# Kernel optimization log

Hardware: AMD Instinct MI355X
Metric: run time of the kernel (lower is better)

Reference implementation:

```python
import jax, jax.numpy as jnp
import numpy as np

N_NODES = 50000
N_EDGES = 800000
N_FIELDS = 4
N_MESH = 8
HIDDEN = 128
IN_CH = N_FIELDS * 1 + N_MESH  # 12


def _w(key, shape, scale=0.05):
    return jax.random.normal(key, shape, dtype=jnp.float32) * scale


def setup_inputs() -> dict:
    key = jax.random.key(0)
    ks = jax.random.split(key, 20)
    inp = {
        "F_0": jax.random.normal(ks[0], (N_NODES, 1, N_FIELDS), dtype=jnp.float32),
        "meshfield": jax.random.normal(ks[1], (N_NODES, N_MESH), dtype=jnp.float32),
        "edge_index": jax.random.randint(ks[2], (2, N_EDGES), 0, N_NODES, dtype=jnp.int32),
        "n_timesteps": 8,
        # encoder SAGEConv 1: in 12 -> 128 ; SAGEConv 2: 128 -> 128
        "enc1_Wl": _w(ks[3], (HIDDEN, IN_CH)), "enc1_bl": jnp.zeros((HIDDEN,), jnp.float32), "enc1_Wr": _w(ks[4], (HIDDEN, IN_CH)),
        "enc2_Wl": _w(ks[5], (HIDDEN, HIDDEN)), "enc2_bl": jnp.zeros((HIDDEN,), jnp.float32), "enc2_Wr": _w(ks[6], (HIDDEN, HIDDEN)),
        # decoder SAGEConv 1 & 2: 128 -> 128
        "dec1_Wl": _w(ks[7], (HIDDEN, HIDDEN)), "dec1_bl": jnp.zeros((HIDDEN,), jnp.float32), "dec1_Wr": _w(ks[8], (HIDDEN, HIDDEN)),
        "dec2_Wl": _w(ks[9], (HIDDEN, HIDDEN)), "dec2_bl": jnp.zeros((HIDDEN,), jnp.float32), "dec2_Wr": _w(ks[10], (HIDDEN, HIDDEN)),
        # output head: 128 -> n_fields
        "lin_W": _w(ks[11], (N_FIELDS, HIDDEN)), "lin_b": jnp.zeros((N_FIELDS,), jnp.float32),
    }
    return inp


def sage_conv(x, src, dst, Wl, bl, Wr, n_nodes):
    # PyG SAGEConv: out = lin_l(mean_j x_j) + lin_r(x_i); lin_l has bias, lin_r does not.
    msg = x[src]                                             # [E, C] gather
    agg = jax.ops.segment_sum(msg, dst, num_segments=n_nodes)
    cnt = jax.ops.segment_sum(jnp.ones((src.shape[0], 1), x.dtype), dst, num_segments=n_nodes)
    agg = agg / jnp.maximum(cnt, 1.0)                        # scatter-mean
    return agg @ Wl.T + bl + x @ Wr.T


def reference(F_0, meshfield, edge_index, n_timesteps,
              enc1_Wl, enc1_bl, enc1_Wr, enc2_Wl, enc2_bl, enc2_Wr,
              dec1_Wl, dec1_bl, dec1_Wr, dec2_Wl, dec2_bl, dec2_Wr,
              lin_W, lin_b):
    n = F_0.shape[0]
    src, dst = edge_index[0], edge_index[1]
    relu = jax.nn.relu
    F_prev = F_0  # [N, n_prev=1, n_fields]
    outs = []
    for _ in range(int(n_timesteps)):
        x_prev = F_prev[:, -1]                               # [N, n_fields]
        x = jnp.concatenate([F_prev.reshape(n, -1), meshfield], axis=1)  # [N, 12]
        # encoder GraphSAGE (act between layers, none after last)
        h = relu(sage_conv(x, src, dst, enc1_Wl, enc1_bl, enc1_Wr, n))
        h = sage_conv(h, src, dst, enc2_Wl, enc2_bl, enc2_Wr, n)
        h = relu(h)                                          # self.act after encoder
        # decoder GraphSAGE
        h = relu(sage_conv(h, src, dst, dec1_Wl, dec1_bl, dec1_Wr, n))
        h = sage_conv(h, src, dst, dec2_Wl, dec2_bl, dec2_Wr, n)
        h = relu(h)                                          # self.act after decoder
        x_new = x_prev + h @ lin_W.T + lin_b                 # residual update
        outs.append(x_new[:, None, :])
        # recurrence uses detached prediction (x.detach() in torch)
        F_prev = jnp.concatenate([F_prev[:, 1:], jax.lax.stop_gradient(x_new)[:, None, :]], axis=1)
    return jnp.concatenate(outs, axis=1)                     # [N, n_timesteps, n_fields]
```

## Files before the change

### kernel.cpp

```cpp
#include <hip/hip_runtime.h>


typedef __attribute__((ext_vector_type(8))) short short8;
typedef __attribute__((ext_vector_type(8))) unsigned short ushort8;
typedef __attribute__((ext_vector_type(4))) float f32x4;

static __device__ __forceinline__ float b2f(unsigned short u) {
  return __uint_as_float(((unsigned int)u) << 16);
}
static __device__ __forceinline__ unsigned short f2bf(float f) {
  unsigned int u = __float_as_uint(f);
  u += 0x7FFFu + ((u >> 16) & 1u);
  return (unsigned short)(u >> 16);
}


__global__ void count_deg_kernel(const int* __restrict__ dst, int* __restrict__ cnt, int E) {
  int e = blockIdx.x * blockDim.x + threadIdx.x;
  if (e < E) atomicAdd(&cnt[dst[e]], 1);
}

__global__ void rdeg_kernel(const int* __restrict__ cnt, float* __restrict__ rdeg, int N) {
  int n = blockIdx.x * blockDim.x + threadIdx.x;
  if (n < N) rdeg[n] = 1.0f / fmaxf((float)cnt[n], 1.0f);
}

__global__ __launch_bounds__(1024) void scan_kernel(const int* __restrict__ cnt,
                                                    int* __restrict__ row_ptr, int n) {
  __shared__ int sums[1024];
  int tid = threadIdx.x;
  int seg = (n + 1023) >> 10;
  int i0 = tid * seg;
  int i1 = i0 + seg; if (i1 > n) i1 = n;
  int s = 0;
  for (int i = i0; i < i1; ++i) s += cnt[i];
  sums[tid] = s;
  __syncthreads();
  for (int off = 1; off < 1024; off <<= 1) {
    int t = (tid >= off) ? sums[tid - off] : 0;
    __syncthreads();
    sums[tid] += t;
    __syncthreads();
  }
  int run = (tid == 0) ? 0 : sums[tid - 1];
  for (int i = i0; i < i1; ++i) { run += cnt[i]; row_ptr[i + 1] = run; }
  if (tid == 0) row_ptr[0] = 0;
}

__global__ void fill_csr_kernel(const int* __restrict__ src, const int* __restrict__ dst,
                                const int* __restrict__ row_ptr, int* __restrict__ cursor,
                                int* __restrict__ col, int E) {
  int e = blockIdx.x * blockDim.x + threadIdx.x;
  if (e < E) {
    int d = dst[e];
    int p = atomicAdd(&cursor[d], 1);
    col[row_ptr[d] + p] = src[e];
  }
}

__global__ void f2bf_kernel(const float* __restrict__ src, unsigned short* __restrict__ dst, int n) {
  int i = blockIdx.x * blockDim.x + threadIdx.x;
  if (i < n) dst[i] = f2bf(src[i]);
}


__global__ void build_xcat_kernel(const float* __restrict__ xprev, const float* __restrict__ mesh,
                                  float* __restrict__ xcat, int N) {
  int g = blockIdx.x * blockDim.x + threadIdx.x;
  if (g < N * 12) {
    int n = g / 12, c = g % 12;
    xcat[g] = (c < 4) ? xprev[n * 4 + c] : mesh[n * 8 + (c - 4)];
  }
}

__global__ void agg12_kernel(const float* __restrict__ feat, float* __restrict__ out,
                             const int* __restrict__ row_ptr, const int* __restrict__ col,
                             const float* __restrict__ rdeg, int N) {
  int g = blockIdx.x * blockDim.x + threadIdx.x;
  int node = g >> 4;
  int d = g & 15;
  if (node >= N || d >= 12) return;
  int j0 = row_ptr[node], j1 = row_ptr[node + 1];
  float acc = 0.0f;
  for (int j = j0; j < j1; ++j) acc += feat[col[j] * 12 + d];
  out[node * 12 + d] = acc * rdeg[node];
}

__global__ void agg128_kernel(const unsigned short* __restrict__ feat,
                              unsigned short* __restrict__ out,
                              const int* __restrict__ row_ptr, const int* __restrict__ col,
                              const float* __restrict__ rdeg, int N) {
  int g = blockIdx.x * blockDim.x + threadIdx.x;
  int node = g >> 4;
  int d = g & 15;
  if (node >= N) return;
  int j0 = row_ptr[node], j1 = row_ptr[node + 1];
  float acc[8] = {};
  int j = j0;
  for (; j + 2 <= j1; j += 2) {
    int s0 = col[j], s1 = col[j + 1];
    ushort8 v0 = *(const ushort8*)&feat[s0 * 128 + d * 8];
    ushort8 v1 = *(const ushort8*)&feat[s1 * 128 + d * 8];
#pragma unroll
    for (int r = 0; r < 8; ++r) acc[r] += b2f(v0[r]) + b2f(v1[r]);
  }
  if (j < j1) {
    ushort8 v0 = *(const ushort8*)&feat[col[j] * 128 + d * 8];
#pragma unroll
    for (int r = 0; r < 8; ++r) acc[r] += b2f(v0[r]);
  }
  float rd = rdeg[node];
  ushort8 o;
#pragma unroll
  for (int r = 0; r < 8; ++r) o[r] = f2bf(acc[r] * rd);
  *(ushort8*)&out[node * 128 + d * 8] = o;
}

__global__ __launch_bounds__(256) void gemm12_kernel(
    const float* __restrict__ agg, const float* __restrict__ x,
    const float* __restrict__ Wl, const float* __restrict__ Wr,
    const float* __restrict__ bl, unsigned short* __restrict__ out, int N) {
  __shared__ float Ws[24][128];
  __shared__ float As[16][24];
  int tid = threadIdx.x;
  int nb = blockIdx.x * 16;
  for (int i = tid; i < 1536; i += 256) {
    int o = i / 12, k = i % 12;
    Ws[k][o] = Wl[i];
    Ws[12 + k][o] = Wr[i];
  }
  for (int i = tid; i < 192; i += 256) {
    int n = i / 12, k = i % 12;
    int gn = nb + n; if (gn > N - 1) gn = N - 1;
    As[n][k] = agg[gn * 12 + k];
    As[n][12 + k] = x[gn * 12 + k];
  }
  __syncthreads();
  int nl = tid >> 4;
  int og = tid & 15;
  float acc[8] = {};
#pragma unroll
  for (int k = 0; k < 24; ++k) {
    float a = As[nl][k];
    float4 w0 = *(const float4*)&Ws[k][og * 8];
    float4 w1 = *(const float4*)&Ws[k][og * 8 + 4];
    acc[0] += a * w0.x; acc[1] += a * w0.y; acc[2] += a * w0.z; acc[3] += a * w0.w;
    acc[4] += a * w1.x; acc[5] += a * w1.y; acc[6] += a * w1.z; acc[7] += a * w1.w;
  }
  int gn = nb + nl;
  if (gn < N) {
#pragma unroll
    for (int j = 0; j < 8; ++j) {
      float v = acc[j] + bl[og * 8 + j];
      out[gn * 128 + og * 8 + j] = f2bf(fmaxf(v, 0.0f));
    }
  }
}

__global__ __launch_bounds__(256) void gemm128_mfma_kernel(
    const unsigned short* __restrict__ agg, const unsigned short* __restrict__ x,
    const unsigned short* __restrict__ Wlb, const unsigned short* __restrict__ Wrb,
    const float* __restrict__ bl, unsigned short* __restrict__ out, int N) {
  int tid = threadIdx.x;
  int wave = tid >> 6;
  int lane = tid & 63;
  int nb = blockIdx.x * 128 + wave * 32;
  int l15 = lane & 15;
  int lk = (lane >> 4) * 8;

  f32x4 acc[2][8] = {};
  int r0 = nb + l15;      if (r0 > N - 1) r0 = N - 1;
  int r1 = nb + 16 + l15; if (r1 > N - 1) r1 = N - 1;

#pragma unroll
  for (int ks = 0; ks < 8; ++ks) {
    const unsigned short* As = (ks < 4) ? agg : x;
    const unsigned short* Ws = (ks < 4) ? Wlb : Wrb;
    int ko = (ks & 3) * 32 + lk;
    short8 a0 = *(const short8*)&As[r0 * 128 + ko];
    short8 a1 = *(const short8*)&As[r1 * 128 + ko];
#pragma unroll
    for (int ot = 0; ot < 8; ++ot) {
      short8 b = *(const short8*)&Ws[(ot * 16 + l15) * 128 + ko];
      acc[0][ot] = __builtin_amdgcn_mfma_f32_16x16x32_bf16(a0, b, acc[0][ot], 0, 0, 0);
      acc[1][ot] = __builtin_amdgcn_mfma_f32_16x16x32_bf16(a1, b, acc[1][ot], 0, 0, 0);
    }
  }

  int crow = (lane >> 4) * 4;
#pragma unroll
  for (int ot = 0; ot < 8; ++ot) {
    int gcol = ot * 16 + l15;
    float bv = bl[gcol];
#pragma unroll
    for (int mt = 0; mt < 2; ++mt) {
#pragma unroll
      for (int r = 0; r < 4; ++r) {
        int grow = nb + mt * 16 + crow + r;
        if (grow < N) {
          float v = fmaxf(acc[mt][ot][r] + bv, 0.0f);
          out[grow * 128 + gcol] = f2bf(v);
        }
      }
    }
  }
}

__global__ __launch_bounds__(256) void lin_kernel(
    const unsigned short* __restrict__ h, const float* __restrict__ linW,
    const float* __restrict__ linb, float* __restrict__ xprev,
    float* __restrict__ out, int N, int T, int t) {
  __shared__ float hs[64][132];
  __shared__ float Wls[4][132];
  int tid = threadIdx.x;
  int nb = blockIdx.x * 64;
  for (int i = tid; i < 512; i += 256) Wls[i >> 7][i & 127] = linW[i];
  for (int i = tid; i < 1024; i += 256) {
    int n = i >> 4, c = i & 15;
    int gn = nb + n; if (gn > N - 1) gn = N - 1;
    ushort8 v = *(const ushort8*)&h[gn * 128 + c * 8];
#pragma unroll
    for (int r = 0; r < 8; ++r) hs[n][c * 8 + r] = b2f(v[r]);
  }
  __syncthreads();
  int nl = tid >> 2, o = tid & 3;
  float acc = 0.0f;
#pragma unroll 8
  for (int k = 0; k < 128; k += 4) {
    float4 hv = *(const float4*)&hs[nl][k];
    float4 wv = *(const float4*)&Wls[o][k];
    acc += hv.x * wv.x + hv.y * wv.y + hv.z * wv.z + hv.w * wv.w;
  }
  int gn = nb + nl;
  if (gn < N) {
    float v = xprev[gn * 4 + o] + acc + linb[o];
    out[(gn * T + t) * 4 + o] = v;
    xprev[gn * 4 + o] = v;
  }
}

extern "C" void kernel_launch(void* const* d_in, const int* in_sizes, int n_in,
                              void* d_out, int out_size, void* d_ws, size_t ws_size,
                              hipStream_t stream) {
  const float* F0   = (const float*)d_in[0];
  const float* mesh = (const float*)d_in[1];
  const int*   eidx = (const int*)d_in[2];
  const float* e1Wl = (const float*)d_in[4];
  const float* e1bl = (const float*)d_in[5];
  const float* e1Wr = (const float*)d_in[6];
  const float* e2Wl = (const float*)d_in[7];
  const float* e2bl = (const float*)d_in[8];
  const float* e2Wr = (const float*)d_in[9];
  const float* d1Wl = (const float*)d_in[10];
  const float* d1bl = (const float*)d_in[11];
  const float* d1Wr = (const float*)d_in[12];
  const float* d2Wl = (const float*)d_in[13];
  const float* d2bl = (const float*)d_in[14];
  const float* d2Wr = (const float*)d_in[15];
  const float* linW = (const float*)d_in[16];
  const float* linb = (const float*)d_in[17];

  const int N = in_sizes[0] / 4;
  const int E = in_sizes[2] / 2;
  const int T = out_size / (N * 4);
  const int* src = eidx;
  const int* dst = eidx + E;

  size_t off = 0;
  auto alloc = [&](size_t bytes) -> void* {
    void* p = (char*)d_ws + off;
    off += (bytes + 511) & ~(size_t)511;
    return p;
  };
  int*   cnt     = (int*)alloc((size_t)N * 4);
  int*   row_ptr = (int*)alloc((size_t)(N + 1) * 4);
  int*   cursor  = (int*)alloc((size_t)N * 4);
  int*   col     = (int*)alloc((size_t)E * 4);
  float* rdeg    = (float*)alloc((size_t)N * 4);
  float* xprev   = (float*)alloc((size_t)N * 4 * 4);
  float* xcat    = (float*)alloc((size_t)N * 12 * 4);
  float* agg12b  = (float*)alloc((size_t)N * 12 * 4);
  unsigned short* h1   = (unsigned short*)alloc((size_t)N * 128 * 2);
  unsigned short* h2   = (unsigned short*)alloc((size_t)N * 128 * 2);
  unsigned short* aggb = (unsigned short*)alloc((size_t)N * 128 * 2);
  unsigned short* wb   = (unsigned short*)alloc((size_t)6 * 128 * 128 * 2);
  unsigned short* e2Wlb = wb + 0 * 16384;
  unsigned short* e2Wrb = wb + 1 * 16384;
  unsigned short* d1Wlb = wb + 2 * 16384;
  unsigned short* d1Wrb = wb + 3 * 16384;
  unsigned short* d2Wlb = wb + 4 * 16384;
  unsigned short* d2Wrb = wb + 5 * 16384;

  float* outp = (float*)d_out;

  hipMemsetAsync(cnt, 0, (size_t)N * 4, stream);
  hipMemsetAsync(cursor, 0, (size_t)N * 4, stream);
  count_deg_kernel<<<(E + 255) / 256, 256, 0, stream>>>(dst, cnt, E);
  rdeg_kernel<<<(N + 255) / 256, 256, 0, stream>>>(cnt, rdeg, N);
  scan_kernel<<<1, 1024, 0, stream>>>(cnt, row_ptr, N);
  fill_csr_kernel<<<(E + 255) / 256, 256, 0, stream>>>(src, dst, row_ptr, cursor, col, E);

  f2bf_kernel<<<64, 256, 0, stream>>>(e2Wl, e2Wlb, 16384);
  f2bf_kernel<<<64, 256, 0, stream>>>(e2Wr, e2Wrb, 16384);
  f2bf_kernel<<<64, 256, 0, stream>>>(d1Wl, d1Wlb, 16384);
  f2bf_kernel<<<64, 256, 0, stream>>>(d1Wr, d1Wrb, 16384);
  f2bf_kernel<<<64, 256, 0, stream>>>(d2Wl, d2Wlb, 16384);
  f2bf_kernel<<<64, 256, 0, stream>>>(d2Wr, d2Wrb, 16384);

  hipMemcpyAsync(xprev, F0, (size_t)N * 4 * 4, hipMemcpyDeviceToDevice, stream);

  const int gAgg128 = (N * 16 + 255) / 256;
  const int gAgg12  = (N * 16 + 255) / 256;
  const int gGemm   = (N + 127) / 128;
  const int gGemm12 = (N + 15) / 16;
  const int gLin    = (N + 63) / 64;

  for (int t = 0; t < T; ++t) {
    build_xcat_kernel<<<(N * 12 + 255) / 256, 256, 0, stream>>>(xprev, mesh, xcat, N);
    agg12_kernel<<<gAgg12, 256, 0, stream>>>(xcat, agg12b, row_ptr, col, rdeg, N);
    gemm12_kernel<<<gGemm12, 256, 0, stream>>>(agg12b, xcat, e1Wl, e1Wr, e1bl, h1, N);

    agg128_kernel<<<gAgg128, 256, 0, stream>>>(h1, aggb, row_ptr, col, rdeg, N);
    gemm128_mfma_kernel<<<gGemm, 256, 0, stream>>>(aggb, h1, e2Wlb, e2Wrb, e2bl, h2, N);

    agg128_kernel<<<gAgg128, 256, 0, stream>>>(h2, aggb, row_ptr, col, rdeg, N);
    gemm128_mfma_kernel<<<gGemm, 256, 0, stream>>>(aggb, h2, d1Wlb, d1Wrb, d1bl, h1, N);

    agg128_kernel<<<gAgg128, 256, 0, stream>>>(h1, aggb, row_ptr, col, rdeg, N);
    gemm128_mfma_kernel<<<gGemm, 256, 0, stream>>>(aggb, h1, d2Wlb, d2Wrb, d2bl, h2, N);

    lin_kernel<<<gLin, 256, 0, stream>>>(h2, linW, linb, xprev, outp, N, T, t);
  }
}
```

Before: 2.013 ms.

## Fuse first-layer aggregation, head projection, parallelize scan, and batch weight conversion

Replaces the single-block CSR scan with a three-stage multi-block scan that also computes reciprocal degrees. The xcat build, 12-channel aggregation and first GEMM are fused into one kernel, and the last SAGE GEMM is fused with the linear head and residual update, so h2 is never written. Weight conversions are batched into one launch and the 128-channel aggregation is unrolled by four for more memory parallelism. This cuts launches and intermediate global traffic, at the cost of more register pressure in the fused head kernel and redundant weight staging in enc1.

After: 1.735 ms. -13.8%, faster.

```diff
diff --git a/kernel.cpp b/kernel.cpp
--- a/kernel.cpp
+++ b/kernel.cpp
@@ -20,31 +20,57 @@
   if (e < E) atomicAdd(&cnt[dst[e]], 1);
 }
 
-__global__ void rdeg_kernel(const int* __restrict__ cnt, float* __restrict__ rdeg, int N) {
-  int n = blockIdx.x * blockDim.x + threadIdx.x;
-  if (n < N) rdeg[n] = 1.0f / fmaxf((float)cnt[n], 1.0f);
-}
-
-__global__ __launch_bounds__(1024) void scan_kernel(const int* __restrict__ cnt,
-                                                    int* __restrict__ row_ptr, int n) {
-  __shared__ int sums[1024];
-  int tid = threadIdx.x;
-  int seg = (n + 1023) >> 10;
-  int i0 = tid * seg;
-  int i1 = i0 + seg; if (i1 > n) i1 = n;
-  int s = 0;
-  for (int i = i0; i < i1; ++i) s += cnt[i];
-  sums[tid] = s;
+__global__ __launch_bounds__(256) void blocksum_kernel(const int* __restrict__ cnt,
+                                                       int* __restrict__ bsum, int n) {
+  __shared__ int s[256];
+  int tid = threadIdx.x;
+  int i = blockIdx.x * 256 + tid;
+  s[tid] = (i < n) ? cnt[i] : 0;
   __syncthreads();
-  for (int off = 1; off < 1024; off <<= 1) {
-    int t = (tid >= off) ? sums[tid - off] : 0;
+  for (int off = 128; off > 0; off >>= 1) {
+    if (tid < off) s[tid] += s[tid + off];
     __syncthreads();
-    sums[tid] += t;
+  }
+  if (tid == 0) bsum[blockIdx.x] = s[0];
+}
+
+__global__ __launch_bounds__(256) void scan_sums_kernel(const int* __restrict__ bsum,
+                                                        int* __restrict__ boff, int nb) {
+  __shared__ int s[256];
+  int tid = threadIdx.x;
+  int v = (tid < nb) ? bsum[tid] : 0;
+  s[tid] = v;
+  __syncthreads();
+  for (int off = 1; off < 256; off <<= 1) {
+    int t = (tid >= off) ? s[tid - off] : 0;
     __syncthreads();
-  }
-  int run = (tid == 0) ? 0 : sums[tid - 1];
-  for (int i = i0; i < i1; ++i) { run += cnt[i]; row_ptr[i + 1] = run; }
-  if (tid == 0) row_ptr[0] = 0;
+    s[tid] += t;
+    __syncthreads();
+  }
+  if (tid < nb) boff[tid] = s[tid] - v;
+}
+
+__global__ __launch_bounds__(256) void expand_kernel(const int* __restrict__ cnt,
+                                                     const int* __restrict__ boff,
+                                                     int* __restrict__ row_ptr,
+                                                     float* __restrict__ rdeg, int n) {
+  __shared__ int s[256];
+  int tid = threadIdx.x;
+  int i = blockIdx.x * 256 + tid;
+  int v = (i < n) ? cnt[i] : 0;
+  s[tid] = v;
+  __syncthreads();
+  for (int off = 1; off < 256; off <<= 1) {
+    int t = (tid >= off) ? s[tid - off] : 0;
+    __syncthreads();
+    s[tid] += t;
+    __syncthreads();
+  }
+  if (i < n) {
+    row_ptr[i + 1] = boff[blockIdx.x] + s[tid];
+    rdeg[i] = 1.0f / fmaxf((float)v, 1.0f);
+  }
+  if (i == 0) row_ptr[0] = 0;
 }
 
 __global__ void fill_csr_kernel(const int* __restrict__ src, const int* __restrict__ dst,
@@ -58,32 +84,77 @@
   }
 }
 
-__global__ void f2bf_kernel(const float* __restrict__ src, unsigned short* __restrict__ dst, int n) {
+__global__ void f2bf6_kernel(const float* __restrict__ s0, const float* __restrict__ s1,
+                             const float* __restrict__ s2, const float* __restrict__ s3,
+                             const float* __restrict__ s4, const float* __restrict__ s5,
+                             unsigned short* __restrict__ dst) {
   int i = blockIdx.x * blockDim.x + threadIdx.x;
-  if (i < n) dst[i] = f2bf(src[i]);
-}
-
-
-__global__ void build_xcat_kernel(const float* __restrict__ xprev, const float* __restrict__ mesh,
-                                  float* __restrict__ xcat, int N) {
-  int g = blockIdx.x * blockDim.x + threadIdx.x;
-  if (g < N * 12) {
-    int n = g / 12, c = g % 12;
-    xcat[g] = (c < 4) ? xprev[n * 4 + c] : mesh[n * 8 + (c - 4)];
-  }
-}
-
-__global__ void agg12_kernel(const float* __restrict__ feat, float* __restrict__ out,
-                             const int* __restrict__ row_ptr, const int* __restrict__ col,
-                             const float* __restrict__ rdeg, int N) {
-  int g = blockIdx.x * blockDim.x + threadIdx.x;
-  int node = g >> 4;
-  int d = g & 15;
-  if (node >= N || d >= 12) return;
-  int j0 = row_ptr[node], j1 = row_ptr[node + 1];
-  float acc = 0.0f;
-  for (int j = j0; j < j1; ++j) acc += feat[col[j] * 12 + d];
-  out[node * 12 + d] = acc * rdeg[node];
+  if (i >= 6 * 16384) return;
+  int m = i >> 14, o = i & 16383;
+  const float* s;
+  switch (m) {
+    case 0: s = s0; break; case 1: s = s1; break; case 2: s = s2; break;
+    case 3: s = s3; break; case 4: s = s4; break; default: s = s5; break;
+  }
+  dst[i] = f2bf(s[o]);
+}
+
+
+__global__ __launch_bounds__(256) void enc1_kernel(
+    const float* __restrict__ xprev, const float* __restrict__ mesh,
+    const int* __restrict__ row_ptr, const int* __restrict__ col,
+    const float* __restrict__ rdeg,
+    const float* __restrict__ Wl, const float* __restrict__ Wr,
+    const float* __restrict__ bl, unsigned short* __restrict__ out, int N) {
+  __shared__ float Ws[24][128];
+  __shared__ float As[16][24];
+  int tid = threadIdx.x;
+  int nb = blockIdx.x * 16;
+  for (int i = tid; i < 1536; i += 256) {
+    int o = i / 12, k = i % 12;
+    Ws[k][o] = Wl[i];
+    Ws[12 + k][o] = Wr[i];
+  }
+  if (tid < 192) {
+    int n = tid / 12, k = tid % 12;
+    int gn = nb + n; if (gn > N - 1) gn = N - 1;
+    float own = (k < 4) ? xprev[gn * 4 + k] : mesh[gn * 8 + (k - 4)];
+    As[n][12 + k] = own;
+    int j0 = row_ptr[gn], j1 = row_ptr[gn + 1];
+    float acc = 0.0f;
+    int j = j0;
+    for (; j + 2 <= j1; j += 2) {
+      int s0 = col[j], s1 = col[j + 1];
+      float v0 = (k < 4) ? xprev[s0 * 4 + k] : mesh[s0 * 8 + (k - 4)];
+      float v1 = (k < 4) ? xprev[s1 * 4 + k] : mesh[s1 * 8 + (k - 4)];
+      acc += v0 + v1;
+    }
+    if (j < j1) {
+      int s0 = col[j];
+      acc += (k < 4) ? xprev[s0 * 4 + k] : mesh[s0 * 8 + (k - 4)];
+    }
+    As[n][k] = acc * rdeg[gn];
+  }
+  __syncthreads();
+  int nl = tid >> 4;
+  int og = tid & 15;
+  float acc[8] = {};
+#pragma unroll
+  for (int k = 0; k < 24; ++k) {
+    float a = As[nl][k];
+    float4 w0 = *(const float4*)&Ws[k][og * 8];
+    float4 w1 = *(const float4*)&Ws[k][og * 8 + 4];
+    acc[0] += a * w0.x; acc[1] += a * w0.y; acc[2] += a * w0.z; acc[3] += a * w0.w;
+    acc[4] += a * w1.x; acc[5] += a * w1.y; acc[6] += a * w1.z; acc[7] += a * w1.w;
+  }
+  int gn = nb + nl;
+  if (gn < N) {
+#pragma unroll
+    for (int j = 0; j < 8; ++j) {
+      float v = acc[j] + bl[og * 8 + j];
+      out[gn * 128 + og * 8 + j] = f2bf(fmaxf(v, 0.0f));
+    }
+  }
 }
 
 __global__ void agg128_kernel(const unsigned short* __restrict__ feat,
@@ -97,14 +168,17 @@
   int j0 = row_ptr[node], j1 = row_ptr[node + 1];
   float acc[8] = {};
   int j = j0;
-  for (; j + 2 <= j1; j += 2) {
-    int s0 = col[j], s1 = col[j + 1];
+  for (; j + 4 <= j1; j += 4) {
+    int s0 = col[j], s1 = col[j + 1], s2 = col[j + 2], s3 = col[j + 3];
     ushort8 v0 = *(const ushort8*)&feat[s0 * 128 + d * 8];
     ushort8 v1 = *(const ushort8*)&feat[s1 * 128 + d * 8];
-#pragma unroll
-    for (int r = 0; r < 8; ++r) acc[r] += b2f(v0[r]) + b2f(v1[r]);
-  }
-  if (j < j1) {
+    ushort8 v2 = *(const ushort8*)&feat[s2 * 128 + d * 8];
+    ushort8 v3 = *(const ushort8*)&feat[s3 * 128 + d * 8];
+#pragma unroll
+    for (int r = 0; r < 8; ++r)
+      acc[r] += (b2f(v0[r]) + b2f(v1[r])) + (b2f(v2[r]) + b2f(v3[r]));
+  }
+  for (; j < j1; ++j) {
     ushort8 v0 = *(const ushort8*)&feat[col[j] * 128 + d * 8];
 #pragma unroll
     for (int r = 0; r < 8; ++r) acc[r] += b2f(v0[r]);
@@ -114,47 +188,6 @@
 #pragma unroll
   for (int r = 0; r < 8; ++r) o[r] = f2bf(acc[r] * rd);
   *(ushort8*)&out[node * 128 + d * 8] = o;
-}
-
-__global__ __launch_bounds__(256) void gemm12_kernel(
-    const float* __restrict__ agg, const float* __restrict__ x,
-    const float* __restrict__ Wl, const float* __restrict__ Wr,
-    const float* __restrict__ bl, unsigned short* __restrict__ out, int N) {
-  __shared__ float Ws[24][128];
-  __shared__ float As[16][24];
-  int tid = threadIdx.x;
-  int nb = blockIdx.x * 16;
-  for (int i = tid; i < 1536; i += 256) {
-    int o = i / 12, k = i % 12;
-    Ws[k][o] = Wl[i];
-    Ws[12 + k][o] = Wr[i];
-  }
-  for (int i = tid; i < 192; i += 256) {
-    int n = i / 12, k = i % 12;
-    int gn = nb + n; if (gn > N - 1) gn = N - 1;
-    As[n][k] = agg[gn * 12 + k];
-    As[n][12 + k] = x[gn * 12 + k];
-  }
-  __syncthreads();
-  int nl = tid >> 4;
-  int og = tid & 15;
-  float acc[8] = {};
-#pragma unroll
-  for (int k = 0; k < 24; ++k) {
-    float a = As[nl][k];
-    float4 w0 = *(const float4*)&Ws[k][og * 8];
-    float4 w1 = *(const float4*)&Ws[k][og * 8 + 4];
-    acc[0] += a * w0.x; acc[1] += a * w0.y; acc[2] += a * w0.z; acc[3] += a * w0.w;
-    acc[4] += a * w1.x; acc[5] += a * w1.y; acc[6] += a * w1.z; acc[7] += a * w1.w;
-  }
-  int gn = nb + nl;
-  if (gn < N) {
-#pragma unroll
-    for (int j = 0; j < 8; ++j) {
-      float v = acc[j] + bl[og * 8 + j];
-      out[gn * 128 + og * 8 + j] = f2bf(fmaxf(v, 0.0f));
-    }
-  }
 }
 
 __global__ __launch_bounds__(256) void gemm128_mfma_kernel(
@@ -206,36 +239,88 @@
   }
 }
 
-__global__ __launch_bounds__(256) void lin_kernel(
-    const unsigned short* __restrict__ h, const float* __restrict__ linW,
+__global__ __launch_bounds__(256) void gemm128_head_mfma_kernel(
+    const unsigned short* __restrict__ agg, const unsigned short* __restrict__ x,
+    const unsigned short* __restrict__ Wlb, const unsigned short* __restrict__ Wrb,
+    const float* __restrict__ bl, const float* __restrict__ linW,
     const float* __restrict__ linb, float* __restrict__ xprev,
     float* __restrict__ out, int N, int T, int t) {
-  __shared__ float hs[64][132];
-  __shared__ float Wls[4][132];
-  int tid = threadIdx.x;
-  int nb = blockIdx.x * 64;
-  for (int i = tid; i < 512; i += 256) Wls[i >> 7][i & 127] = linW[i];
-  for (int i = tid; i < 1024; i += 256) {
-    int n = i >> 4, c = i & 15;
-    int gn = nb + n; if (gn > N - 1) gn = N - 1;
-    ushort8 v = *(const ushort8*)&h[gn * 128 + c * 8];
-#pragma unroll
-    for (int r = 0; r < 8; ++r) hs[n][c * 8 + r] = b2f(v[r]);
-  }
+  __shared__ float Wh[4][128];
+  int tid = threadIdx.x;
+  for (int i = tid; i < 512; i += 256) Wh[i >> 7][i & 127] = linW[i];
   __syncthreads();
-  int nl = tid >> 2, o = tid & 3;
-  float acc = 0.0f;
-#pragma unroll 8
-  for (int k = 0; k < 128; k += 4) {
-    float4 hv = *(const float4*)&hs[nl][k];
-    float4 wv = *(const float4*)&Wls[o][k];
-    acc += hv.x * wv.x + hv.y * wv.y + hv.z * wv.z + hv.w * wv.w;
-  }
-  int gn = nb + nl;
-  if (gn < N) {
-    float v = xprev[gn * 4 + o] + acc + linb[o];
-    out[(gn * T + t) * 4 + o] = v;
-    xprev[gn * 4 + o] = v;
+
+  int wave = tid >> 6;
+  int lane = tid & 63;
+  int nb = blockIdx.x * 128 + wave * 32;
+  int l15 = lane & 15;
+  int lk = (lane >> 4) * 8;
+
+  f32x4 acc[2][8] = {};
+  int r0 = nb + l15;      if (r0 > N - 1) r0 = N - 1;
+  int r1 = nb + 16 + l15; if (r1 > N - 1) r1 = N - 1;
+
+#pragma unroll
+  for (int ks = 0; ks < 8; ++ks) {
+    const unsigned short* As = (ks < 4) ? agg : x;
+    const unsigned short* Ws = (ks < 4) ? Wlb : Wrb;
+    int ko = (ks & 3) * 32 + lk;
+    short8 a0 = *(const short8*)&As[r0 * 128 + ko];
+    short8 a1 = *(const short8*)&As[r1 * 128 + ko];
+#pragma unroll
+    for (int ot = 0; ot < 8; ++ot) {
+      short8 b = *(const short8*)&Ws[(ot * 16 + l15) * 128 + ko];
+      acc[0][ot] = __builtin_amdgcn_mfma_f32_16x16x32_bf16(a0, b, acc[0][ot], 0, 0, 0);
+      acc[1][ot] = __builtin_amdgcn_mfma_f32_16x16x32_bf16(a1, b, acc[1][ot], 0, 0, 0);
+    }
+  }
+
+  float part[2][4][4] = {};
+#pragma unroll
+  for (int ot = 0; ot < 8; ++ot) {
+    int gcol = ot * 16 + l15;
+    float bv = bl[gcol];
+    float w0 = Wh[0][gcol], w1 = Wh[1][gcol], w2 = Wh[2][gcol], w3 = Wh[3][gcol];
+#pragma unroll
+    for (int mt = 0; mt < 2; ++mt)
+#pragma unroll
+      for (int r = 0; r < 4; ++r) {
+        float hv = fmaxf(acc[mt][ot][r] + bv, 0.0f);
+        part[mt][r][0] += hv * w0;
+        part[mt][r][1] += hv * w1;
+        part[mt][r][2] += hv * w2;
+        part[mt][r][3] += hv * w3;
+      }
+  }
+#pragma unroll
+  for (int m = 1; m < 16; m <<= 1)
+#pragma unroll
+    for (int mt = 0; mt < 2; ++mt)
+#pragma unroll
+      for (int r = 0; r < 4; ++r)
+#pragma unroll
+        for (int o = 0; o < 4; ++o)
+          part[mt][r][o] += __shfl_xor(part[mt][r][o], m, 64);
+
+  if (l15 == 0) {
+    int crow = (lane >> 4) * 4;
+    float4 lb = *(const float4*)linb;
+#pragma unroll
+    for (int mt = 0; mt < 2; ++mt)
+#pragma unroll
+      for (int r = 0; r < 4; ++r) {
+        int grow = nb + mt * 16 + crow + r;
+        if (grow < N) {
+          float4 xp = *(const float4*)&xprev[grow * 4];
+          float4 xn;
+          xn.x = xp.x + part[mt][r][0] + lb.x;
+          xn.y = xp.y + part[mt][r][1] + lb.y;
+          xn.z = xp.z + part[mt][r][2] + lb.z;
+          xn.w = xp.w + part[mt][r][3] + lb.w;
+          *(float4*)&out[(grow * T + t) * 4] = xn;
+          *(float4*)&xprev[grow * 4] = xn;
+        }
+      }
   }
 }
 
@@ -278,8 +363,8 @@
   int*   col     = (int*)alloc((size_t)E * 4);
   float* rdeg    = (float*)alloc((size_t)N * 4);
   float* xprev   = (float*)alloc((size_t)N * 4 * 4);
-  float* xcat    = (float*)alloc((size_t)N * 12 * 4);
-  float* agg12b  = (float*)alloc((size_t)N * 12 * 4);
+  int*   bsum    = (int*)alloc(256 * 4);
+  int*   boff    = (int*)alloc(256 * 4);
   unsigned short* h1   = (unsigned short*)alloc((size_t)N * 128 * 2);
   unsigned short* h2   = (unsigned short*)alloc((size_t)N * 128 * 2);
   unsigned short* aggb = (unsigned short*)alloc((size_t)N * 128 * 2);
@@ -293,42 +378,35 @@
 
   float* outp = (float*)d_out;
 
+  const int NB = (N + 255) / 256;
+
   hipMemsetAsync(cnt, 0, (size_t)N * 4, stream);
   hipMemsetAsync(cursor, 0, (size_t)N * 4, stream);
   count_deg_kernel<<<(E + 255) / 256, 256, 0, stream>>>(dst, cnt, E);
-  rdeg_kernel<<<(N + 255) / 256, 256, 0, stream>>>(cnt, rdeg, N);
-  scan_kernel<<<1, 1024, 0, stream>>>(cnt, row_ptr, N);
+  blocksum_kernel<<<NB, 256, 0, stream>>>(cnt, bsum, N);
+  scan_sums_kernel<<<1, 256, 0, stream>>>(bsum, boff, NB);
+  expand_kernel<<<NB, 256, 0, stream>>>(cnt, boff, row_ptr, rdeg, N);
   fill_csr_kernel<<<(E + 255) / 256, 256, 0, stream>>>(src, dst, row_ptr, cursor, col, E);
-
-  f2bf_kernel<<<64, 256, 0, stream>>>(e2Wl, e2Wlb, 16384);
-  f2bf_kernel<<<64, 256, 0, stream>>>(e2Wr, e2Wrb, 16384);
-  f2bf_kernel<<<64, 256, 0, stream>>>(d1Wl, d1Wlb, 16384);
-  f2bf_kernel<<<64, 256, 0, stream>>>(d1Wr, d1Wrb, 16384);
-  f2bf_kernel<<<64, 256, 0, stream>>>(d2Wl, d2Wlb, 16384);
-  f2bf_kernel<<<64, 256, 0, stream>>>(d2Wr, d2Wrb, 16384);
-
+  f2bf6_kernel<<<(6 * 16384 + 255) / 256, 256, 0, stream>>>(
+      e2Wl, e2Wr, d1Wl, d1Wr, d2Wl, d2Wr, wb);
   hipMemcpyAsync(xprev, F0, (size_t)N * 4 * 4, hipMemcpyDeviceToDevice, stream);
 
-  const int gAgg128 = (N * 16 + 255) / 256;
-  const int gAgg12  = (N * 16 + 255) / 256;
-  const int gGemm   = (N + 127) / 128;
-  const int gGemm12 = (N + 15) / 16;
-  const int gLin    = (N + 63) / 64;
+  const int gAgg  = (N * 16 + 255) / 256;
+  const int gGemm = (N + 127) / 128;
+  const int gEnc1 = (N + 15) / 16;
 
   for (int t = 0; t < T; ++t) {
-    build_xcat_kernel<<<(N * 12 + 255) / 256, 256, 0, stream>>>(xprev, mesh, xcat, N);
-    agg12_kernel<<<gAgg12, 256, 0, stream>>>(xcat, agg12b, row_ptr, col, rdeg, N);
-    gemm12_kernel<<<gGemm12, 256, 0, stream>>>(agg12b, xcat, e1Wl, e1Wr, e1bl, h1, N);
-
-    agg128_kernel<<<gAgg128, 256, 0, stream>>>(h1, aggb, row_ptr, col, rdeg, N);
+    enc1_kernel<<<gEnc1, 256, 0, stream>>>(xprev, mesh, row_ptr, col, rdeg,
+                                           e1Wl, e1Wr, e1bl, h1, N);
+
+    agg128_kernel<<<gAgg, 256, 0, stream>>>(h1, aggb, row_ptr, col, rdeg, N);
     gemm128_mfma_kernel<<<gGemm, 256, 0, stream>>>(aggb, h1, e2Wlb, e2Wrb, e2bl, h2, N);
 
-    agg128_kernel<<<gAgg128, 256, 0, stream>>>(h2, aggb, row_ptr, col, rdeg, N);
+    agg128_kernel<<<gAgg, 256, 0, stream>>>(h2, aggb, row_ptr, col, rdeg, N);
     gemm128_mfma_kernel<<<gGemm, 256, 0, stream>>>(aggb, h2, d1Wlb, d1Wrb, d1bl, h1, N);
 
-    agg128_kernel<<<gAgg128, 256, 0, stream>>>(h1, aggb, row_ptr, col, rdeg, N);
-    gemm128_mfma_kernel<<<gGemm, 256, 0, stream>>>(aggb, h1, d2Wlb, d2Wrb, d2bl, h2, N);
-
-    lin_kernel<<<gLin, 256, 0, stream>>>(h2, linW, linb, xprev, outp, N, T, t);
-  }
-}
+    agg128_kernel<<<gAgg, 256, 0, stream>>>(h1, aggb, row_ptr, col, rdeg, N);
+    gemm128_head_mfma_kernel<<<gGemm, 256, 0, stream>>>(aggb, h1, d2Wlb, d2Wrb, d2bl,
+                                                        linW, linb, xprev, outp, N, T, t);
+  }
+}
```
